# Kernel tuning notes

Hardware: AMD Instinct MI355X
Metric: run time of the kernel (lower is better)

The kernel has to match this reference:

```python
import jax, jax.numpy as jnp
import numpy as np

# dims matching init_kwargs
E = 256        # obs dim
H = 128        # rnn_hidden_dim
NQ = 8         # n_quantiles (forward_type='policy')
QED = 64       # quantile_embed_dim
HEADS = 2      # hpn_head_num
HYP = 64       # hpn_hyper_dim
NA = 14        # n_actions
NAG = 8        # n_agents
B = 512        # episode batch


def setup_inputs() -> dict:
    key = jax.random.key(0)
    ks = jax.random.split(key, 16)
    def rn(k, shape, scale):
        return jax.random.normal(k, shape, dtype=jnp.float32) * scale
    inp = {
        "inputs": rn(ks[0], (B, NAG, E), 1.0),
        "hidden_state": rn(ks[1], (B * NAG, H), 1.0),
        "rnd_quantiles": jax.random.uniform(ks[2], (B, 1, NQ), dtype=jnp.float32),
        # fc1
        "fc1_w": rn(ks[3], (E, H), 1.0 / np.sqrt(E)),
        "fc1_b": jnp.zeros((H,), jnp.float32),
        # hypernet (2-layer MLP producing per-sample H x (H*HEADS) weights)
        "hyp_w1": rn(ks[4], (NQ, HYP), 1.0 / np.sqrt(NQ)),
        "hyp_b1": jnp.zeros((HYP,), jnp.float32),
        "hyp_w2": rn(ks[5], (HYP, H * H * HEADS), 1.0 / np.sqrt(HYP)),
        "hyp_b2": jnp.zeros((H * H * HEADS,), jnp.float32),
        # merger softmax weights [1, heads, H], init 1.0 as in module
        "merger_w": jnp.ones((1, HEADS, H), jnp.float32),
        # GRUCell params (PyTorch layout: [3H, in])
        "gru_wi": rn(ks[6], (3 * H, H), 1.0 / np.sqrt(H)),
        "gru_wh": rn(ks[7], (3 * H, H), 1.0 / np.sqrt(H)),
        "gru_bi": jnp.zeros((3 * H,), jnp.float32),
        "gru_bh": jnp.zeros((3 * H,), jnp.float32),
        # phi (quantile embedding linear)
        "phi_w": rn(ks[8], (QED, H), 1.0 / np.sqrt(QED)),
        "phi_b": jnp.zeros((H,), jnp.float32),
        # fc2
        "fc2_w": rn(ks[9], (H, NA), 1.0 / np.sqrt(H)),
        "fc2_b": jnp.zeros((NA,), jnp.float32),
    }
    return inp


def reference(inputs, hidden_state, rnd_quantiles, fc1_w, fc1_b,
              hyp_w1, hyp_b1, hyp_w2, hyp_b2, merger_w,
              gru_wi, gru_wh, gru_bi, gru_bh, phi_w, phi_b, fc2_w, fc2_b):
    b, a, e = inputs.shape
    bs = b * a
    # fc1 + relu
    x = jax.nn.relu(inputs.reshape(bs, e) @ fc1_w + fc1_b)          # [bs, H]
    # prev return distribution: first-call value = ones
    prev = jnp.ones((bs, NQ), dtype=inputs.dtype)
    # hypernet -> per-sample weights [bs, H, H*HEADS]
    hh = jax.nn.relu(prev @ hyp_w1 + hyp_b1)
    input_w = (hh @ hyp_w2 + hyp_b2).reshape(bs, H, H * HEADS)
    # batched matmul: [bs,1,H] @ [bs,H,H*HEADS] -> [bs, HEADS, H]
    emb = jnp.einsum('bi,bio->bo', x, input_w).reshape(bs, HEADS, H)
    # merger: softmax over head dim
    emb = jnp.sum(jax.nn.softmax(merger_w, axis=1) * emb, axis=1)   # [bs, H]
    x2 = jax.nn.relu(emb)
    # GRUCell (PyTorch semantics)
    hprev = hidden_state.reshape(-1, H)
    gi = x2 @ gru_wi.T + gru_bi
    gh = hprev @ gru_wh.T + gru_bh
    ir, iz, inn = jnp.split(gi, 3, axis=1)
    hr, hz, hn = jnp.split(gh, 3, axis=1)
    r = jax.nn.sigmoid(ir + hr)
    z = jax.nn.sigmoid(iz + hz)
    n = jnp.tanh(inn + r * hn)
    h = (1.0 - z) * n + z * hprev                                   # [bs, H]
    # IQN quantile embedding (forward_type='policy', grouped by agents)
    nq = NQ
    bsg = bs // NAG
    rq = rnd_quantiles.reshape(-1)                                  # [bsg*nq]
    h2 = jnp.broadcast_to(h[:, None, :], (bs, nq, H)).reshape(bs * nq, H)
    fid = jnp.arange(QED, dtype=inputs.dtype)                       # [QED]
    cos = jnp.cos(jnp.pi * fid[None, :] * rq[:, None])              # [bsg*nq, QED]
    q_phi = jax.nn.relu(cos @ phi_w + phi_b)                        # [bsg*nq, H]
    q_phi = jnp.broadcast_to(q_phi.reshape(bsg, 1, nq, H),
                             (bsg, NAG, nq, H)).reshape(bs * nq, H)
    q = (h2 * q_phi) @ fc2_w + fc2_b                                # [bs*nq, NA]
    q = q.reshape(bs, nq, NA).transpose(0, 2, 1)                    # [bs, NA, nq]
    sorted_q = jnp.sort(q, axis=2)
    return sorted_q, h, rq.reshape(bsg, nq)
```

## Files before the change

kernel.cpp:

```cpp
#include <hip/hip_runtime.h>
#include <math.h>

typedef __attribute__((ext_vector_type(8))) short short8;
typedef __attribute__((ext_vector_type(4))) float floatx4;

#define E_DIM 256
#define H_DIM 128
#define NQv 8
#define QEDv 64
#define HYPv 64
#define NAv 14
#define NAGv 8
#define W2COL 32768

#define OUT_H_OFF 458752
#define OUT_RQ_OFF 983040

#define FB_W1  0
#define FB_WE  4096
#define FB_WI  6144
#define FB_WH  12288
#define FB_PHI 18432
#define FB_FC2 19456
#define PACK_UNITS 17664

#define SM_IN   0
#define SM_X1   8192
#define SM_X2   12288
#define SM_H    16384
#define SM_PART 0
#define SM_HF   32768
#define SM_QP   41216
#define SM_TOTAL 45568

__device__ __forceinline__ unsigned short f2bf(float x) {
  unsigned u = __builtin_bit_cast(unsigned, x);
  u += 0x7FFFu + ((u >> 16) & 1u);
  return (unsigned short)(u >> 16);
}
__device__ __forceinline__ float bf2f(unsigned short s) {
  return __builtin_bit_cast(float, ((unsigned)s) << 16);
}

__global__ __launch_bounds__(256) void k_weff(
    const float* __restrict__ hyp_w1, const float* __restrict__ hyp_b1,
    const float* __restrict__ hyp_w2, const float* __restrict__ hyp_b2,
    const float* __restrict__ merger_w, unsigned short* __restrict__ wp) {
  __shared__ float hh[HYPv];
  __shared__ float part[4][2][64];
  int t = threadIdx.x;
  if (t < HYPv) {
    float s = hyp_b1[t];
#pragma unroll
    for (int i = 0; i < NQv; ++i) s += hyp_w1[i * HYPv + t];
    hh[t] = fmaxf(s, 0.f);
  }
  __syncthreads();
  int w = t >> 6, lane = t & 63;
  int i = blockIdx.x >> 1;
  int cbase = (blockIdx.x & 1) * 64;
  int o0 = i * 256 + cbase + lane;
  float a0 = 0.f, a1 = 0.f;
#pragma unroll
  for (int jj = 0; jj < 16; ++jj) {
    int j = w * 16 + jj;
    float hj = hh[j];
    a0 = fmaf(hj, hyp_w2[j * W2COL + o0], a0);
    a1 = fmaf(hj, hyp_w2[j * W2COL + o0 + 128], a1);
  }
  part[w][0][lane] = a0;
  part[w][1][lane] = a1;
  __syncthreads();
  if (t < 64) {
    int c = cbase + t;
    float h0 = part[0][0][t] + part[1][0][t] + part[2][0][t] + part[3][0][t]
               + hyp_b2[i * 256 + c];
    float h1 = part[0][1][t] + part[1][1][t] + part[2][1][t] + part[3][1][t]
               + hyp_b2[i * 256 + c + 128];
    float m0 = merger_w[c], m1 = merger_w[128 + c];
    float mx = fmaxf(m0, m1);
    float e0 = expf(m0 - mx), e1 = expf(m1 - mx);
    float val = (e0 * h0 + e1 * h1) / (e0 + e1);
    int unit = FB_WE + ((i >> 5) * 8 + (c >> 4)) * 64 + ((i >> 3) & 3) * 16 + (c & 15);
    wp[(size_t)unit * 8 + (i & 7)] = f2bf(val);
  }
}

__global__ __launch_bounds__(256) void k_pack(
    const float* __restrict__ fc1_w, const float* __restrict__ gru_wi,
    const float* __restrict__ gru_wh, const float* __restrict__ phi_w,
    const float* __restrict__ fc2_w, unsigned short* __restrict__ wp) {
  int u = blockIdx.x * 256 + threadIdx.x;
  if (u >= PACK_UNITS) return;
  float v[8];
  int f;
  if (u < 4096) {
    int g = u, nt = (g >> 6) & 7, lane = g & 63;
    int k0 = (g >> 9) * 32 + ((lane >> 4) << 3), n = nt * 16 + (lane & 15);
    f = FB_W1 + g;
#pragma unroll
    for (int j = 0; j < 8; ++j) v[j] = fc1_w[(k0 + j) * H_DIM + n];
  } else if (u < 10240) {
    int g = u - 4096, kt = g / 1536, rem = g % 1536, nt = rem >> 6, lane = rem & 63;
    int k0 = kt * 32 + ((lane >> 4) << 3), n = nt * 16 + (lane & 15);
    f = FB_WI + g;
#pragma unroll
    for (int j = 0; j < 8; ++j) v[j] = gru_wi[n * H_DIM + k0 + j];
  } else if (u < 16384) {
    int g = u - 10240, kt = g / 1536, rem = g % 1536, nt = rem >> 6, lane = rem & 63;
    int k0 = kt * 32 + ((lane >> 4) << 3), n = nt * 16 + (lane & 15);
    f = FB_WH + g;
#pragma unroll
    for (int j = 0; j < 8; ++j) v[j] = gru_wh[n * H_DIM + k0 + j];
  } else if (u < 17408) {
    int g = u - 16384, kt = g >> 9, nt = (g >> 6) & 7, lane = g & 63;
    int k0 = kt * 32 + ((lane >> 4) << 3), n = nt * 16 + (lane & 15);
    f = FB_PHI + g;
#pragma unroll
    for (int j = 0; j < 8; ++j) v[j] = phi_w[(k0 + j) * H_DIM + n];
  } else {
    int g = u - 17408, kt = g >> 6, lane = g & 63;
    int k0 = kt * 32 + ((lane >> 4) << 3), n = lane & 15;
    f = FB_FC2 + g;
#pragma unroll
    for (int j = 0; j < 8; ++j) v[j] = (n < NAv) ? fc2_w[(k0 + j) * NAv + n] : 0.f;
  }
  short8 pk;
#pragma unroll
  for (int j = 0; j < 8; ++j) pk[j] = (short)f2bf(v[j]);
  *(short8*)(wp + (size_t)f * 8) = pk;
}

__global__ __launch_bounds__(256) void k_main(
    const float* __restrict__ inp, const float* __restrict__ hprev,
    const float* __restrict__ rnd, const float* __restrict__ fc1_b,
    const unsigned short* __restrict__ wp,
    const float* __restrict__ gru_bi, const float* __restrict__ gru_bh,
    const float* __restrict__ phi_b, const float* __restrict__ fc2_b,
    float* __restrict__ h_out, float* __restrict__ q_out,
    float* __restrict__ rq_out) {
  __shared__ __align__(16) char smem[SM_TOTAL];
  unsigned short (*lds_in)[64][8] = (unsigned short(*)[64][8])(smem + SM_IN);
  unsigned short (*lds_x1)[64][8] = (unsigned short(*)[64][8])(smem + SM_X1);
  unsigned short (*lds_x2)[64][8] = (unsigned short(*)[64][8])(smem + SM_X2);
  unsigned short (*lds_h)[64][8]  = (unsigned short(*)[64][8])(smem + SM_H);
  float (*lds_hf)[132]            = (float(*)[132])(smem + SM_HF);
  unsigned short (*lds_qp)[136]   = (unsigned short(*)[136])(smem + SM_QP);
  float* lds_part                 = (float*)(smem + SM_PART);

  int t = threadIdx.x;
  int b0 = blockIdx.x * 16;
  int lane = t & 63, w = t >> 6;
  int quad = lane >> 4, l16 = lane & 15;

  if (t < 16) rq_out[b0 + t] = rnd[b0 + t];

#pragma unroll
  for (int i = 0; i < 2; ++i) {
    int idx = i * 256 + t;
    int oct = idx & 31, m = idx >> 5;
    const float* p = inp + (size_t)(b0 + m) * E_DIM + oct * 8;
    floatx4 v0 = *(const floatx4*)p;
    floatx4 v1 = *(const floatx4*)(p + 4);
    short8 pk;
    pk[0] = (short)f2bf(v0.x); pk[1] = (short)f2bf(v0.y);
    pk[2] = (short)f2bf(v0.z); pk[3] = (short)f2bf(v0.w);
    pk[4] = (short)f2bf(v1.x); pk[5] = (short)f2bf(v1.y);
    pk[6] = (short)f2bf(v1.z); pk[7] = (short)f2bf(v1.w);
    *(short8*)&lds_in[oct >> 2][(oct & 3) * 16 + m][0] = pk;
  }
  {
    int oct = t & 15, m = t >> 4;
    const float* p = hprev + (size_t)(b0 + m) * H_DIM + oct * 8;
    floatx4 v0 = *(const floatx4*)p;
    floatx4 v1 = *(const floatx4*)(p + 4);
    short8 pk;
    pk[0] = (short)f2bf(v0.x); pk[1] = (short)f2bf(v0.y);
    pk[2] = (short)f2bf(v0.z); pk[3] = (short)f2bf(v0.w);
    pk[4] = (short)f2bf(v1.x); pk[5] = (short)f2bf(v1.y);
    pk[6] = (short)f2bf(v1.z); pk[7] = (short)f2bf(v1.w);
    *(short8*)&lds_h[oct >> 2][(oct & 3) * 16 + m][0] = pk;
  }

  {
    float rqv = rnd[b0 + l16];
    short8 aC[2];
#pragma unroll
    for (int kt = 0; kt < 2; ++kt) {
#pragma unroll
      for (int j = 0; j < 8; ++j) {
        float f = (float)(kt * 32 + quad * 8 + j);
        aC[kt][j] = (short)f2bf(__cosf(3.14159265358979f * f * rqv));
      }
    }
    floatx4 cP[2] = {{0.f,0.f,0.f,0.f},{0.f,0.f,0.f,0.f}};
#pragma unroll
    for (int kt = 0; kt < 2; ++kt) {
#pragma unroll
      for (int ni = 0; ni < 2; ++ni) {
        int nt = w * 2 + ni;
        short8 b = *(const short8*)(wp + ((size_t)(FB_PHI + (kt * 8 + nt) * 64 + lane)) * 8);
        cP[ni] = __builtin_amdgcn_mfma_f32_16x16x32_bf16(aC[kt], b, cP[ni], 0, 0, 0);
      }
    }
#pragma unroll
    for (int ni = 0; ni < 2; ++ni) {
      int col = (w * 2 + ni) * 16 + l16;
      float bias = phi_b[col];
#pragma unroll
      for (int reg = 0; reg < 4; ++reg) {
        int m_qp = quad * 4 + reg;
        lds_qp[m_qp][col] = f2bf(fmaxf(cP[ni][reg] + bias, 0.f));
      }
    }
  }
  __syncthreads();

  int nt0 = w * 2;
  {
    short8 aIn[8];
#pragma unroll
    for (int kt = 0; kt < 8; ++kt)
      aIn[kt] = *(const short8*)&lds_in[kt][lane][0];
    floatx4 c1[2] = {{0.f,0.f,0.f,0.f},{0.f,0.f,0.f,0.f}};
#pragma unroll
    for (int kt = 0; kt < 8; ++kt) {
#pragma unroll
      for (int n = 0; n < 2; ++n) {
        short8 b = *(const short8*)(wp + ((size_t)(FB_W1 + (kt * 8 + nt0 + n) * 64 + lane)) * 8);
        c1[n] = __builtin_amdgcn_mfma_f32_16x16x32_bf16(aIn[kt], b, c1[n], 0, 0, 0);
      }
    }
#pragma unroll
    for (int n = 0; n < 2; ++n) {
      int col = (nt0 + n) * 16 + l16;
      float bias = fc1_b[col];
#pragma unroll
      for (int reg = 0; reg < 4; ++reg) {
        float v = fmaxf(c1[n][reg] + bias, 0.f);
        lds_x1[col >> 5][((col >> 3) & 3) * 16 + quad * 4 + reg][col & 7] = f2bf(v);
      }
    }
  }
  __syncthreads();

  {
    short8 a2[4];
#pragma unroll
    for (int kt = 0; kt < 4; ++kt)
      a2[kt] = *(const short8*)&lds_x1[kt][lane][0];
    floatx4 c2[2] = {{0.f,0.f,0.f,0.f},{0.f,0.f,0.f,0.f}};
#pragma unroll
    for (int kt = 0; kt < 4; ++kt) {
#pragma unroll
      for (int n = 0; n < 2; ++n) {
        short8 b = *(const short8*)(wp + ((size_t)(FB_WE + (kt * 8 + nt0 + n) * 64 + lane)) * 8);
        c2[n] = __builtin_amdgcn_mfma_f32_16x16x32_bf16(a2[kt], b, c2[n], 0, 0, 0);
      }
    }
#pragma unroll
    for (int n = 0; n < 2; ++n) {
      int col = (nt0 + n) * 16 + l16;
#pragma unroll
      for (int reg = 0; reg < 4; ++reg) {
        float v = fmaxf(c2[n][reg], 0.f);
        lds_x2[col >> 5][((col >> 3) & 3) * 16 + quad * 4 + reg][col & 7] = f2bf(v);
      }
    }
  }
  __syncthreads();

  {
    short8 ax[4], ah[4];
#pragma unroll
    for (int kt = 0; kt < 4; ++kt) {
      ax[kt] = *(const short8*)&lds_x2[kt][lane][0];
      ah[kt] = *(const short8*)&lds_h[kt][lane][0];
    }
#pragma unroll
    for (int cti = 0; cti < 2; ++cti) {
      int ct = w + cti * 4;
      floatx4 giR = {0.f,0.f,0.f,0.f}, giZ = {0.f,0.f,0.f,0.f}, giN = {0.f,0.f,0.f,0.f};
      floatx4 ghR = {0.f,0.f,0.f,0.f}, ghZ = {0.f,0.f,0.f,0.f}, ghN = {0.f,0.f,0.f,0.f};
#pragma unroll
      for (int kt = 0; kt < 4; ++kt) {
        short8 bR = *(const short8*)(wp + ((size_t)(FB_WI + (kt * 24 + ct) * 64 + lane)) * 8);
        short8 bZ = *(const short8*)(wp + ((size_t)(FB_WI + (kt * 24 + ct + 8) * 64 + lane)) * 8);
        short8 bN = *(const short8*)(wp + ((size_t)(FB_WI + (kt * 24 + ct + 16) * 64 + lane)) * 8);
        short8 cR = *(const short8*)(wp + ((size_t)(FB_WH + (kt * 24 + ct) * 64 + lane)) * 8);
        short8 cZ = *(const short8*)(wp + ((size_t)(FB_WH + (kt * 24 + ct + 8) * 64 + lane)) * 8);
        short8 cN = *(const short8*)(wp + ((size_t)(FB_WH + (kt * 24 + ct + 16) * 64 + lane)) * 8);
        giR = __builtin_amdgcn_mfma_f32_16x16x32_bf16(ax[kt], bR, giR, 0, 0, 0);
        giZ = __builtin_amdgcn_mfma_f32_16x16x32_bf16(ax[kt], bZ, giZ, 0, 0, 0);
        giN = __builtin_amdgcn_mfma_f32_16x16x32_bf16(ax[kt], bN, giN, 0, 0, 0);
        ghR = __builtin_amdgcn_mfma_f32_16x16x32_bf16(ah[kt], cR, ghR, 0, 0, 0);
        ghZ = __builtin_amdgcn_mfma_f32_16x16x32_bf16(ah[kt], cZ, ghZ, 0, 0, 0);
        ghN = __builtin_amdgcn_mfma_f32_16x16x32_bf16(ah[kt], cN, ghN, 0, 0, 0);
      }
      int c = ct * 16 + l16;
      float bir = gru_bi[c], biz = gru_bi[128 + c], bin = gru_bi[256 + c];
      float bhr = gru_bh[c], bhz = gru_bh[128 + c], bhn = gru_bh[256 + c];
#pragma unroll
      for (int reg = 0; reg < 4; ++reg) {
        int rl = quad * 4 + reg;
        int row = b0 + rl;
        float r = 1.f / (1.f + expf(-(giR[reg] + bir + ghR[reg] + bhr)));
        float z = 1.f / (1.f + expf(-(giZ[reg] + biz + ghZ[reg] + bhz)));
        float n = tanhf(giN[reg] + bin + r * (ghN[reg] + bhn));
        float hp = hprev[(size_t)row * H_DIM + c];
        float hv = (1.f - z) * n + z * hp;
        h_out[(size_t)row * H_DIM + c] = hv;
        lds_hf[rl][c] = hv;
      }
    }
  }
  __syncthreads();

  {
    int m = l16;
    int k0 = w * 32 + quad * 8;
    const float* hptr = &lds_hf[m][k0];
    floatx4 h0 = *(const floatx4*)hptr;
    floatx4 h1 = *(const floatx4*)(hptr + 4);
    float hf[8] = {h0.x, h0.y, h0.z, h0.w, h1.x, h1.y, h1.z, h1.w};
    short8 bF = *(const short8*)(wp + ((size_t)(FB_FC2 + w * 64 + lane)) * 8);
    int qbase = (m >> 3) * 8;
    floatx4 cQ[8];
#pragma unroll
    for (int q = 0; q < NQv; ++q) cQ[q] = (floatx4){0.f,0.f,0.f,0.f};
#pragma unroll
    for (int q = 0; q < NQv; ++q) {
      short8 qpv = *(const short8*)&lds_qp[qbase + q][k0];
      short8 au;
#pragma unroll
      for (int j = 0; j < 8; ++j)
        au[j] = (short)f2bf(hf[j] * bf2f((unsigned short)qpv[j]));
      cQ[q] = __builtin_amdgcn_mfma_f32_16x16x32_bf16(au, bF, cQ[q], 0, 0, 0);
    }
#pragma unroll
    for (int q = 0; q < NQv; ++q)
      *(floatx4*)&lds_part[((w * 8 + q) * 64 + lane) * 4] = cQ[q];
  }
  __syncthreads();

  {
    int s = t >> 4, a = t & 15;
    int pl = (s >> 2) * 16 + a;
    int pr = s & 3;
    float bias = (a < NAv) ? fc2_b[a] : 0.f;
    float qv[NQv];
#pragma unroll
    for (int q = 0; q < NQv; ++q) {
      float acc = bias;
#pragma unroll
      for (int ww = 0; ww < 4; ++ww)
        acc += lds_part[((ww * 8 + q) * 64 + pl) * 4 + pr];
      qv[q] = acc;
    }
#define CE(i, j) { float lo_ = fminf(qv[i], qv[j]); float hi_ = fmaxf(qv[i], qv[j]); qv[i] = lo_; qv[j] = hi_; }
    CE(0,1) CE(2,3) CE(4,5) CE(6,7)
    CE(0,2) CE(1,3) CE(4,6) CE(5,7)
    CE(1,2) CE(5,6)
    CE(0,4) CE(1,5) CE(2,6) CE(3,7)
    CE(2,4) CE(3,5)
    CE(1,2) CE(3,4) CE(5,6)
#undef CE
    if (a < NAv) {
      float4* o4 = (float4*)(q_out + (size_t)((b0 + s) * NAv + a) * NQv);
      o4[0] = make_float4(qv[0], qv[1], qv[2], qv[3]);
      o4[1] = make_float4(qv[4], qv[5], qv[6], qv[7]);
    }
  }
}

extern "C" void kernel_launch(void* const* d_in, const int* in_sizes, int n_in,
                              void* d_out, int out_size, void* d_ws, size_t ws_size,
                              hipStream_t stream) {
  (void)in_sizes; (void)n_in; (void)out_size; (void)ws_size;
  const float* inp      = (const float*)d_in[0];
  const float* hidden   = (const float*)d_in[1];
  const float* rnd      = (const float*)d_in[2];
  const float* fc1_w    = (const float*)d_in[3];
  const float* fc1_b    = (const float*)d_in[4];
  const float* hyp_w1   = (const float*)d_in[5];
  const float* hyp_b1   = (const float*)d_in[6];
  const float* hyp_w2   = (const float*)d_in[7];
  const float* hyp_b2   = (const float*)d_in[8];
  const float* merger_w = (const float*)d_in[9];
  const float* gru_wi   = (const float*)d_in[10];
  const float* gru_wh   = (const float*)d_in[11];
  const float* gru_bi   = (const float*)d_in[12];
  const float* gru_bh   = (const float*)d_in[13];
  const float* phi_w    = (const float*)d_in[14];
  const float* phi_b    = (const float*)d_in[15];
  const float* fc2_w    = (const float*)d_in[16];
  const float* fc2_b    = (const float*)d_in[17];
  float* out  = (float*)d_out;
  unsigned short* wp = (unsigned short*)d_ws;
  float* h_out = out + OUT_H_OFF;

  k_pack<<<dim3(69), dim3(256), 0, stream>>>(fc1_w, gru_wi, gru_wh, phi_w,
                                             fc2_w, wp);
  k_weff<<<dim3(256), dim3(256), 0, stream>>>(hyp_w1, hyp_b1, hyp_w2, hyp_b2,
                                              merger_w, wp);
  k_main<<<dim3(256), dim3(256), 0, stream>>>(inp, hidden, rnd, fc1_b, wp,
                                              gru_bi, gru_bh, phi_b, fc2_b,
                                              h_out, out, out + OUT_RQ_OFF);
}
```

Measured before the change: 109.4 us.

## Merge weight-prep kernels, prefetch B fragments into registers, use fast GRU activations

Folds the bf16 weight packing kernel and the hypernetwork effective-weight kernel into a single launch, with a block-index split between the two jobs. This removes one kernel launch and the serialization gap between them. k_main now loads the phi, fc1 and hypernet weight fragments into registers at kernel start, so the global loads overlap the input staging instead of sitting inside the MFMA loops. The GRU sigmoid and tanh are switched to __expf-based approximations, which raises register pressure and slightly changes numerical accuracy.

```diff
diff --git a/kernel.cpp b/kernel.cpp
--- a/kernel.cpp
+++ b/kernel.cpp
@@ -23,6 +23,8 @@
 #define FB_PHI 18432
 #define FB_FC2 19456
 #define PACK_UNITS 17664
+#define PACK_BLOCKS 69
+#define WEFF_BLOCKS 256
 
 #define SM_IN   0
 #define SM_X1   8192
@@ -41,14 +43,69 @@
 __device__ __forceinline__ float bf2f(unsigned short s) {
   return __builtin_bit_cast(float, ((unsigned)s) << 16);
 }
-
-__global__ __launch_bounds__(256) void k_weff(
+__device__ __forceinline__ float fsigmoid(float x) {
+  return 1.f / (1.f + __expf(-x));
+}
+__device__ __forceinline__ float ftanh(float x) {
+  float t = __expf(-2.f * x);
+  return (1.f - t) / (1.f + t);
+}
+
+__global__ __launch_bounds__(256) void k_prep(
+    const float* __restrict__ fc1_w, const float* __restrict__ gru_wi,
+    const float* __restrict__ gru_wh, const float* __restrict__ phi_w,
+    const float* __restrict__ fc2_w,
     const float* __restrict__ hyp_w1, const float* __restrict__ hyp_b1,
     const float* __restrict__ hyp_w2, const float* __restrict__ hyp_b2,
     const float* __restrict__ merger_w, unsigned short* __restrict__ wp) {
   __shared__ float hh[HYPv];
   __shared__ float part[4][2][64];
   int t = threadIdx.x;
+
+  if (blockIdx.x < PACK_BLOCKS) {
+    int u = blockIdx.x * 256 + t;
+    if (u >= PACK_UNITS) return;
+    float v[8];
+    int f;
+    if (u < 4096) {
+      int g = u, nt = (g >> 6) & 7, lane = g & 63;
+      int k0 = (g >> 9) * 32 + ((lane >> 4) << 3), n = nt * 16 + (lane & 15);
+      f = FB_W1 + g;
+#pragma unroll
+      for (int j = 0; j < 8; ++j) v[j] = fc1_w[(k0 + j) * H_DIM + n];
+    } else if (u < 10240) {
+      int g = u - 4096, kt = g / 1536, rem = g % 1536, nt = rem >> 6, lane = rem & 63;
+      int k0 = kt * 32 + ((lane >> 4) << 3), n = nt * 16 + (lane & 15);
+      f = FB_WI + g;
+#pragma unroll
+      for (int j = 0; j < 8; ++j) v[j] = gru_wi[n * H_DIM + k0 + j];
+    } else if (u < 16384) {
+      int g = u - 10240, kt = g / 1536, rem = g % 1536, nt = rem >> 6, lane = rem & 63;
+      int k0 = kt * 32 + ((lane >> 4) << 3), n = nt * 16 + (lane & 15);
+      f = FB_WH + g;
+#pragma unroll
+      for (int j = 0; j < 8; ++j) v[j] = gru_wh[n * H_DIM + k0 + j];
+    } else if (u < 17408) {
+      int g = u - 16384, kt = g >> 9, nt = (g >> 6) & 7, lane = g & 63;
+      int k0 = kt * 32 + ((lane >> 4) << 3), n = nt * 16 + (lane & 15);
+      f = FB_PHI + g;
+#pragma unroll
+      for (int j = 0; j < 8; ++j) v[j] = phi_w[(k0 + j) * H_DIM + n];
+    } else {
+      int g = u - 17408, kt = g >> 6, lane = g & 63;
+      int k0 = kt * 32 + ((lane >> 4) << 3), n = lane & 15;
+      f = FB_FC2 + g;
+#pragma unroll
+      for (int j = 0; j < 8; ++j) v[j] = (n < NAv) ? fc2_w[(k0 + j) * NAv + n] : 0.f;
+    }
+    short8 pk;
+#pragma unroll
+    for (int j = 0; j < 8; ++j) pk[j] = (short)f2bf(v[j]);
+    *(short8*)(wp + (size_t)f * 8) = pk;
+    return;
+  }
+
+  int blk = blockIdx.x - PACK_BLOCKS;
   if (t < HYPv) {
     float s = hyp_b1[t];
 #pragma unroll
@@ -57,8 +114,8 @@
   }
   __syncthreads();
   int w = t >> 6, lane = t & 63;
-  int i = blockIdx.x >> 1;
-  int cbase = (blockIdx.x & 1) * 64;
+  int i = blk >> 1;
+  int cbase = (blk & 1) * 64;
   int o0 = i * 256 + cbase + lane;
   float a0 = 0.f, a1 = 0.f;
 #pragma unroll
@@ -84,51 +141,6 @@
     int unit = FB_WE + ((i >> 5) * 8 + (c >> 4)) * 64 + ((i >> 3) & 3) * 16 + (c & 15);
     wp[(size_t)unit * 8 + (i & 7)] = f2bf(val);
   }
-}
-
-__global__ __launch_bounds__(256) void k_pack(
-    const float* __restrict__ fc1_w, const float* __restrict__ gru_wi,
-    const float* __restrict__ gru_wh, const float* __restrict__ phi_w,
-    const float* __restrict__ fc2_w, unsigned short* __restrict__ wp) {
-  int u = blockIdx.x * 256 + threadIdx.x;
-  if (u >= PACK_UNITS) return;
-  float v[8];
-  int f;
-  if (u < 4096) {
-    int g = u, nt = (g >> 6) & 7, lane = g & 63;
-    int k0 = (g >> 9) * 32 + ((lane >> 4) << 3), n = nt * 16 + (lane & 15);
-    f = FB_W1 + g;
-#pragma unroll
-    for (int j = 0; j < 8; ++j) v[j] = fc1_w[(k0 + j) * H_DIM + n];
-  } else if (u < 10240) {
-    int g = u - 4096, kt = g / 1536, rem = g % 1536, nt = rem >> 6, lane = rem & 63;
-    int k0 = kt * 32 + ((lane >> 4) << 3), n = nt * 16 + (lane & 15);
-    f = FB_WI + g;
-#pragma unroll
-    for (int j = 0; j < 8; ++j) v[j] = gru_wi[n * H_DIM + k0 + j];
-  } else if (u < 16384) {
-    int g = u - 10240, kt = g / 1536, rem = g % 1536, nt = rem >> 6, lane = rem & 63;
-    int k0 = kt * 32 + ((lane >> 4) << 3), n = nt * 16 + (lane & 15);
-    f = FB_WH + g;
-#pragma unroll
-    for (int j = 0; j < 8; ++j) v[j] = gru_wh[n * H_DIM + k0 + j];
-  } else if (u < 17408) {
-    int g = u - 16384, kt = g >> 9, nt = (g >> 6) & 7, lane = g & 63;
-    int k0 = kt * 32 + ((lane >> 4) << 3), n = nt * 16 + (lane & 15);
-    f = FB_PHI + g;
-#pragma unroll
-    for (int j = 0; j < 8; ++j) v[j] = phi_w[(k0 + j) * H_DIM + n];
-  } else {
-    int g = u - 17408, kt = g >> 6, lane = g & 63;
-    int k0 = kt * 32 + ((lane >> 4) << 3), n = lane & 15;
-    f = FB_FC2 + g;
-#pragma unroll
-    for (int j = 0; j < 8; ++j) v[j] = (n < NAv) ? fc2_w[(k0 + j) * NAv + n] : 0.f;
-  }
-  short8 pk;
-#pragma unroll
-  for (int j = 0; j < 8; ++j) pk[j] = (short)f2bf(v[j]);
-  *(short8*)(wp + (size_t)f * 8) = pk;
 }
 
 __global__ __launch_bounds__(256) void k_main(
@@ -152,6 +164,27 @@
   int b0 = blockIdx.x * 16;
   int lane = t & 63, w = t >> 6;
   int quad = lane >> 4, l16 = lane & 15;
+  int nt0 = w * 2;
+
+  short8 bPhi[2][2], bW1[8][2], bWE[4][2];
+#pragma unroll
+  for (int kt = 0; kt < 2; ++kt)
+#pragma unroll
+    for (int ni = 0; ni < 2; ++ni)
+      bPhi[kt][ni] = *(const short8*)(wp +
+          ((size_t)(FB_PHI + (kt * 8 + nt0 + ni) * 64 + lane)) * 8);
+#pragma unroll
+  for (int kt = 0; kt < 8; ++kt)
+#pragma unroll
+    for (int ni = 0; ni < 2; ++ni)
+      bW1[kt][ni] = *(const short8*)(wp +
+          ((size_t)(FB_W1 + (kt * 8 + nt0 + ni) * 64 + lane)) * 8);
+#pragma unroll
+  for (int kt = 0; kt < 4; ++kt)
+#pragma unroll
+    for (int ni = 0; ni < 2; ++ni)
+      bWE[kt][ni] = *(const short8*)(wp +
+          ((size_t)(FB_WE + (kt * 8 + nt0 + ni) * 64 + lane)) * 8);
 
   if (t < 16) rq_out[b0 + t] = rnd[b0 + t];
 
@@ -195,17 +228,13 @@
     }
     floatx4 cP[2] = {{0.f,0.f,0.f,0.f},{0.f,0.f,0.f,0.f}};
 #pragma unroll
-    for (int kt = 0; kt < 2; ++kt) {
-#pragma unroll
-      for (int ni = 0; ni < 2; ++ni) {
-        int nt = w * 2 + ni;
-        short8 b = *(const short8*)(wp + ((size_t)(FB_PHI + (kt * 8 + nt) * 64 + lane)) * 8);
-        cP[ni] = __builtin_amdgcn_mfma_f32_16x16x32_bf16(aC[kt], b, cP[ni], 0, 0, 0);
-      }
-    }
+    for (int kt = 0; kt < 2; ++kt)
+#pragma unroll
+      for (int ni = 0; ni < 2; ++ni)
+        cP[ni] = __builtin_amdgcn_mfma_f32_16x16x32_bf16(aC[kt], bPhi[kt][ni], cP[ni], 0, 0, 0);
 #pragma unroll
     for (int ni = 0; ni < 2; ++ni) {
-      int col = (w * 2 + ni) * 16 + l16;
+      int col = (nt0 + ni) * 16 + l16;
       float bias = phi_b[col];
 #pragma unroll
       for (int reg = 0; reg < 4; ++reg) {
@@ -216,7 +245,6 @@
   }
   __syncthreads();
 
-  int nt0 = w * 2;
   {
     short8 aIn[8];
 #pragma unroll
@@ -224,13 +252,10 @@
       aIn[kt] = *(const short8*)&lds_in[kt][lane][0];
     floatx4 c1[2] = {{0.f,0.f,0.f,0.f},{0.f,0.f,0.f,0.f}};
 #pragma unroll
-    for (int kt = 0; kt < 8; ++kt) {
-#pragma unroll
-      for (int n = 0; n < 2; ++n) {
-        short8 b = *(const short8*)(wp + ((size_t)(FB_W1 + (kt * 8 + nt0 + n) * 64 + lane)) * 8);
-        c1[n] = __builtin_amdgcn_mfma_f32_16x16x32_bf16(aIn[kt], b, c1[n], 0, 0, 0);
-      }
-    }
+    for (int kt = 0; kt < 8; ++kt)
+#pragma unroll
+      for (int n = 0; n < 2; ++n)
+        c1[n] = __builtin_amdgcn_mfma_f32_16x16x32_bf16(aIn[kt], bW1[kt][n], c1[n], 0, 0, 0);
 #pragma unroll
     for (int n = 0; n < 2; ++n) {
       int col = (nt0 + n) * 16 + l16;
@@ -251,13 +276,10 @@
       a2[kt] = *(const short8*)&lds_x1[kt][lane][0];
     floatx4 c2[2] = {{0.f,0.f,0.f,0.f},{0.f,0.f,0.f,0.f}};
 #pragma unroll
-    for (int kt = 0; kt < 4; ++kt) {
-#pragma unroll
-      for (int n = 0; n < 2; ++n) {
-        short8 b = *(const short8*)(wp + ((size_t)(FB_WE + (kt * 8 + nt0 + n) * 64 + lane)) * 8);
-        c2[n] = __builtin_amdgcn_mfma_f32_16x16x32_bf16(a2[kt], b, c2[n], 0, 0, 0);
-      }
-    }
+    for (int kt = 0; kt < 4; ++kt)
+#pragma unroll
+      for (int n = 0; n < 2; ++n)
+        c2[n] = __builtin_amdgcn_mfma_f32_16x16x32_bf16(a2[kt], bWE[kt][n], c2[n], 0, 0, 0);
 #pragma unroll
     for (int n = 0; n < 2; ++n) {
       int col = (nt0 + n) * 16 + l16;
@@ -304,9 +326,9 @@
       for (int reg = 0; reg < 4; ++reg) {
         int rl = quad * 4 + reg;
         int row = b0 + rl;
-        float r = 1.f / (1.f + expf(-(giR[reg] + bir + ghR[reg] + bhr)));
-        float z = 1.f / (1.f + expf(-(giZ[reg] + biz + ghZ[reg] + bhz)));
-        float n = tanhf(giN[reg] + bin + r * (ghN[reg] + bhn));
+        float r = fsigmoid(giR[reg] + bir + ghR[reg] + bhr);
+        float z = fsigmoid(giZ[reg] + biz + ghZ[reg] + bhz);
+        float n = ftanh(giN[reg] + bin + r * (ghN[reg] + bhn));
         float hp = hprev[(size_t)row * H_DIM + c];
         float hv = (1.f - z) * n + z * hp;
         h_out[(size_t)row * H_DIM + c] = hv;
@@ -399,10 +421,9 @@
   unsigned short* wp = (unsigned short*)d_ws;
   float* h_out = out + OUT_H_OFF;
 
-  k_pack<<<dim3(69), dim3(256), 0, stream>>>(fc1_w, gru_wi, gru_wh, phi_w,
-                                             fc2_w, wp);
-  k_weff<<<dim3(256), dim3(256), 0, stream>>>(hyp_w1, hyp_b1, hyp_w2, hyp_b2,
-                                              merger_w, wp);
+  k_prep<<<dim3(PACK_BLOCKS + WEFF_BLOCKS), dim3(256), 0, stream>>>(
+      fc1_w, gru_wi, gru_wh, phi_w, fc2_w,
+      hyp_w1, hyp_b1, hyp_w2, hyp_b2, merger_w, wp);
   k_main<<<dim3(256), dim3(256), 0, stream>>>(inp, hidden, rnd, fc1_b, wp,
                                               gru_bi, gru_bh, phi_b, fc2_b,
                                               h_out, out, out + OUT_RQ_OFF);
```

After: 107.2 us. -2.1%, faster.
